# Kernel optimization log

Hardware: AMD Instinct MI355X
Metric: run time of the kernel (lower is better)

The kernel has to match this reference:

```python
import jax, jax.numpy as jnp
import numpy as np

N = 4096
FIN = 256
FOUT = 256
H = 1  # num_heads MUST be 1: edge projections reshape [N,N,H] -> (1,N,N)
NEG_MASK = -1000000.0
LRELU_SLOPE = 0.2
ESP = 1e-06
LN_EPS = 1e-05


def setup_inputs() -> dict:
    key = jax.random.key(0)
    ks = jax.random.split(key, 9)
    nodes_features = jax.random.normal(ks[0], (N, FIN), dtype=jnp.float32)
    degree_matrix = jax.random.normal(ks[1], (N, N), dtype=jnp.float32)
    edges_features_distance = jax.random.uniform(ks[2], (N, N), dtype=jnp.float32)
    edges_features_bond = jax.random.uniform(ks[3], (N, N), dtype=jnp.float32)
    # learned parameters (xavier-ish scale)
    proj_param = jax.random.normal(ks[4], (H, FIN, FOUT), dtype=jnp.float32) * (1.0 / np.sqrt(FIN))
    a_src = jax.random.normal(ks[5], (H, FOUT, 1), dtype=jnp.float32) * (1.0 / np.sqrt(FOUT))
    a_tgt = jax.random.normal(ks[6], (H, FOUT, 1), dtype=jnp.float32) * (1.0 / np.sqrt(FOUT))
    w_dist = jax.random.normal(ks[7], (H, 1), dtype=jnp.float32)  # nn.Linear(1, H).weight
    w_bond = jax.random.normal(ks[8], (H, 1), dtype=jnp.float32)
    return {
        "nodes_features": nodes_features,
        "degree_matrix": degree_matrix,
        "edges_features_distance": edges_features_distance,
        "edges_features_bond": edges_features_bond,
        "proj_param": proj_param,
        "a_src": a_src,
        "a_tgt": a_tgt,
        "w_dist": w_dist,
        "w_bond": w_bond,
        "cutoff": 0,
    }


def reference(nodes_features, degree_matrix, edges_features_distance,
              edges_features_bond, proj_param, a_src, a_tgt, w_dist, w_bond,
              cutoff=0):
    n = nodes_features.shape[0]
    h, fin, fout = proj_param.shape
    # connectivity mask: keep degree where positive, else large negative
    connectivity_mask = jnp.where(degree_matrix > 0, degree_matrix, NEG_MASK)
    # node projection: [H, N, Fout] (dropout is identity in eval)
    proj = jnp.einsum('nf,hfo->hno', nodes_features, proj_param)
    # attention scores: outer-sum of per-node source/target scores
    s_src = jnp.einsum('hno,hoi->hni', proj, a_src)      # [H, N, 1]
    s_tgt = jnp.einsum('hno,hoi->hni', proj, a_tgt)      # [H, N, 1]
    all_scores = jax.nn.leaky_relu(s_src + jnp.swapaxes(s_tgt, 1, 2), LRELU_SLOPE)  # [H,N,N]
    # edge contributions: Linear(1, H) on scalar edge features, reshaped (1,N,N) (H==1)
    dist_c = ((-edges_features_distance)[..., None] * w_dist[:, 0]).reshape(1, n, n)
    bond_c = (edges_features_bond[..., None] * w_bond[:, 0]).reshape(1, n, n)
    all_scores = all_scores + dist_c + bond_c
    # masked softmax over neighbors
    attn = jax.nn.softmax(all_scores + connectivity_mask[None], axis=-1)  # [H,N,N]
    # weighted aggregation
    out = jnp.einsum('hnm,hmo->hno', attn, proj)  # [H, N, Fout]
    # faithful to torch: transpose(2,1) -> [H,Fout,N] then contiguous view(-1,H,Fout)
    out = jnp.transpose(out, (0, 2, 1)).reshape(-1, h, fout)
    # concat heads (skip connection and bias are disabled per init args)
    out = out.reshape(-1, h * fout)
    out = jax.nn.elu(out)  # ELU activation, alpha=1
    # ---- no_grad connectivity update ----
    o = jax.lax.stop_gradient(out)
    dm = jax.lax.stop_gradient(degree_matrix)
    sim = o @ o.T                                        # [N, N]
    decay = -jax.lax.stop_gradient(edges_features_distance)
    upd = jax.nn.sigmoid(sim) * decay * (dm > 0).astype(o.dtype)
    upd = upd + ESP
    mean = jnp.mean(upd, axis=-1, keepdims=True)
    var = jnp.mean(jnp.square(upd - mean), axis=-1, keepdims=True)
    upd = (upd - mean) / jnp.sqrt(var + LN_EPS)          # layer_norm, no affine
    upd = upd + upd.T
    return out, upd
```

## Files before the change

kernel.cpp:

```cpp
#include <hip/hip_runtime.h>


using f32x4  = __attribute__((ext_vector_type(4))) float;
using bf16x8 = __attribute__((ext_vector_type(8))) __bf16;
using bf16x4 = __attribute__((ext_vector_type(4))) __bf16;
using u32x4  = __attribute__((ext_vector_type(4))) unsigned int;

__global__ __launch_bounds__(256) void cvt_nodes_kernel(const float* __restrict__ x,
                                                        __bf16* __restrict__ y) {
  int i = (blockIdx.x * 256 + threadIdx.x) * 4;
  f32x4 v = *(const f32x4*)(x + i);
  bf16x4 o = { (__bf16)v[0], (__bf16)v[1], (__bf16)v[2], (__bf16)v[3] };
  *(bf16x4*)(y + i) = o;
}

__global__ __launch_bounds__(256) void cvt_wt_kernel(const float* __restrict__ w,
                                                     __bf16* __restrict__ wt) {
  int i = blockIdx.x * 256 + threadIdx.x;
  int o = i >> 8, f = i & 255;
  wt[i] = (__bf16)w[f * 256 + o];
}

template<int BM, int BN, int MODE>
__global__ __launch_bounds__(256) void gemm_bf16_kernel(
    const __bf16* __restrict__ A, const __bf16* __restrict__ Bt,
    int M, int N, int K,
    float* __restrict__ outf, __bf16* __restrict__ outb,
    const float* __restrict__ e0, const float* __restrict__ e1,
    float* __restrict__ outt)
{
  constexpr int LDT = 72;
  constexpr int MI = BM / 32;
  constexpr int NI = BN / 32;
  __shared__ alignas(16) __bf16 As[BM * LDT];
  __shared__ alignas(16) __bf16 Bs[BN * LDT];
  const int tid  = threadIdx.x;
  const int lane = tid & 63;
  const int wid  = tid >> 6;
  const int wm0  = (wid >> 1) * (BM / 2);
  const int wn0  = (wid & 1) * (BN / 2);
  const int m0   = blockIdx.x * BM;
  const int n0   = blockIdx.y * BN;
  const int lr   = lane & 15;
  const int lk   = lane >> 4;

  f32x4 acc[MI][NI];
#pragma unroll
  for (int a = 0; a < MI; ++a)
#pragma unroll
    for (int b = 0; b < NI; ++b) acc[a][b] = (f32x4){0.f, 0.f, 0.f, 0.f};

  for (int kt = 0; kt < K; kt += 64) {
    __syncthreads();
    for (int idx = tid; idx < BM * 8; idx += 256) {
      int r = idx >> 3, c = idx & 7;
      u32x4 v = *(const u32x4*)(A + (size_t)(m0 + r) * K + kt + c * 8);
      *(u32x4*)(As + r * LDT + c * 8) = v;
    }
    for (int idx = tid; idx < BN * 8; idx += 256) {
      int r = idx >> 3, c = idx & 7;
      u32x4 v = *(const u32x4*)(Bt + (size_t)(n0 + r) * K + kt + c * 8);
      *(u32x4*)(Bs + r * LDT + c * 8) = v;
    }
    __syncthreads();
#pragma unroll
    for (int kk = 0; kk < 2; ++kk) {
      bf16x8 av[MI], bv[NI];
#pragma unroll
      for (int mi = 0; mi < MI; ++mi)
        av[mi] = *(const bf16x8*)(As + (wm0 + mi * 16 + lr) * LDT + kk * 32 + lk * 8);
#pragma unroll
      for (int ni = 0; ni < NI; ++ni)
        bv[ni] = *(const bf16x8*)(Bs + (wn0 + ni * 16 + lr) * LDT + kk * 32 + lk * 8);
#pragma unroll
      for (int mi = 0; mi < MI; ++mi)
#pragma unroll
        for (int ni = 0; ni < NI; ++ni)
          acc[mi][ni] = __builtin_amdgcn_mfma_f32_16x16x32_bf16(av[mi], bv[ni], acc[mi][ni], 0, 0, 0);
    }
  }

#pragma unroll
  for (int mi = 0; mi < MI; ++mi) {
#pragma unroll
    for (int ni = 0; ni < NI; ++ni) {
#pragma unroll
      for (int j = 0; j < 4; ++j) {
        const int m = m0 + wm0 + mi * 16 + lk * 4 + j;
        const int n = n0 + wn0 + ni * 16 + lr;
        const float v = acc[mi][ni][j];
        if constexpr (MODE == 0) {
          outf[(size_t)m * 256 + n] = v;
          outb[(size_t)n * 4096 + m] = (__bf16)v;
        } else {
          const size_t idx = (size_t)m * 4096 + n;
          const float d = e0[idx];
          const float g = e1[idx];
          const float s = 1.0f / (1.0f + expf(-v));
          outt[idx] = s * (-d) * (g > 0.f ? 1.0f : 0.0f) + 1e-6f;
        }
      }
    }
  }
}

__global__ __launch_bounds__(256) void gemm_splitk_kernel(
    const __bf16* __restrict__ A, const __bf16* __restrict__ Bt,
    float* __restrict__ partial)
{
  constexpr int LDT = 72;
  __shared__ alignas(16) __bf16 As[64 * LDT];
  __shared__ alignas(16) __bf16 Bs[64 * LDT];
  const int tid  = threadIdx.x;
  const int lane = tid & 63;
  const int wid  = tid >> 6;
  const int wm0  = (wid >> 1) * 32;
  const int wn0  = (wid & 1) * 32;
  const int m0   = blockIdx.x * 64;
  const int n0   = blockIdx.y * 64;
  const int s    = blockIdx.z;
  const int lr   = lane & 15;
  const int lk   = lane >> 4;

  f32x4 acc[2][2];
#pragma unroll
  for (int a = 0; a < 2; ++a)
#pragma unroll
    for (int b = 0; b < 2; ++b) acc[a][b] = (f32x4){0.f, 0.f, 0.f, 0.f};

  const int k0 = s * 512;
  for (int kt = k0; kt < k0 + 512; kt += 64) {
    __syncthreads();
    for (int idx = tid; idx < 512; idx += 256) {
      int r = idx >> 3, c = idx & 7;
      u32x4 v = *(const u32x4*)(A + (size_t)(m0 + r) * 4096 + kt + c * 8);
      *(u32x4*)(As + r * LDT + c * 8) = v;
    }
    for (int idx = tid; idx < 512; idx += 256) {
      int r = idx >> 3, c = idx & 7;
      u32x4 v = *(const u32x4*)(Bt + (size_t)(n0 + r) * 4096 + kt + c * 8);
      *(u32x4*)(Bs + r * LDT + c * 8) = v;
    }
    __syncthreads();
#pragma unroll
    for (int kk = 0; kk < 2; ++kk) {
      bf16x8 av[2], bv[2];
#pragma unroll
      for (int mi = 0; mi < 2; ++mi)
        av[mi] = *(const bf16x8*)(As + (wm0 + mi * 16 + lr) * LDT + kk * 32 + lk * 8);
#pragma unroll
      for (int ni = 0; ni < 2; ++ni)
        bv[ni] = *(const bf16x8*)(Bs + (wn0 + ni * 16 + lr) * LDT + kk * 32 + lk * 8);
#pragma unroll
      for (int mi = 0; mi < 2; ++mi)
#pragma unroll
        for (int ni = 0; ni < 2; ++ni)
          acc[mi][ni] = __builtin_amdgcn_mfma_f32_16x16x32_bf16(av[mi], bv[ni], acc[mi][ni], 0, 0, 0);
    }
  }

  float* P = partial + (size_t)s * (4096 * 256);
#pragma unroll
  for (int mi = 0; mi < 2; ++mi)
#pragma unroll
    for (int ni = 0; ni < 2; ++ni)
#pragma unroll
      for (int j = 0; j < 4; ++j) {
        const int m = m0 + wm0 + mi * 16 + lk * 4 + j;
        const int n = n0 + wn0 + ni * 16 + lr;
        P[(size_t)m * 256 + n] = acc[mi][ni][j];
      }
}

__global__ __launch_bounds__(256) void reduce_elu_kernel(
    const float* __restrict__ partial, float* __restrict__ out0,
    __bf16* __restrict__ E)
{
  __shared__ float tile[64][65];
  const int tid = threadIdx.x;
  const int m0 = blockIdx.x * 64;
  const int n0 = blockIdx.y * 64;
#pragma unroll
  for (int i = 0; i < 4; ++i) {
    int lin = i * 1024 + tid * 4;
    int r = lin >> 6, c = lin & 63;
    f32x4 sum = (f32x4){0.f, 0.f, 0.f, 0.f};
#pragma unroll
    for (int s = 0; s < 8; ++s)
      sum += *(const f32x4*)(partial + (size_t)s * (4096 * 256) +
                             (size_t)(m0 + r) * 256 + n0 + c);
    tile[r][c]     = sum[0];
    tile[r][c + 1] = sum[1];
    tile[r][c + 2] = sum[2];
    tile[r][c + 3] = sum[3];
  }
  __syncthreads();
#pragma unroll
  for (int i = 0; i < 4; ++i) {
    int lin = i * 1024 + tid * 4;
    int rr = lin >> 6, cc = lin & 63;
    f32x4 e;
#pragma unroll
    for (int q = 0; q < 4; ++q) {
      float v = tile[cc + q][rr];
      e[q] = v > 0.f ? v : expm1f(v);
    }
    size_t idx = (size_t)(n0 + rr) * 4096 + m0 + cc;
    *(f32x4*)(out0 + idx) = e;
    bf16x4 eb = { (__bf16)e[0], (__bf16)e[1], (__bf16)e[2], (__bf16)e[3] };
    *(bf16x4*)(E + idx) = eb;
  }
}

__global__ __launch_bounds__(256) void sproj_kernel(const float* __restrict__ proj,
                                                    const float* __restrict__ asrc,
                                                    const float* __restrict__ atgt,
                                                    float* __restrict__ ssrc,
                                                    float* __restrict__ stgt) {
  const int row  = blockIdx.x * 4 + (threadIdx.x >> 6);
  const int lane = threadIdx.x & 63;
  f32x4 p = *(const f32x4*)(proj + (size_t)row * 256 + lane * 4);
  f32x4 a = *(const f32x4*)(asrc + lane * 4);
  f32x4 b = *(const f32x4*)(atgt + lane * 4);
  float d1 = p[0]*a[0] + p[1]*a[1] + p[2]*a[2] + p[3]*a[3];
  float d2 = p[0]*b[0] + p[1]*b[1] + p[2]*b[2] + p[3]*b[3];
#pragma unroll
  for (int o = 32; o; o >>= 1) { d1 += __shfl_xor(d1, o, 64); d2 += __shfl_xor(d2, o, 64); }
  if (lane == 0) { ssrc[row] = d1; stgt[row] = d2; }
}

__global__ __launch_bounds__(256, 4) void scores_kernel(
    const float* __restrict__ dist, const float* __restrict__ bond,
    const float* __restrict__ deg,  const float* __restrict__ ssrc,
    const float* __restrict__ stgt, const float* __restrict__ wdp,
    const float* __restrict__ wbp,  __bf16* __restrict__ attn)
{
  const int row = blockIdx.x;
  const int tid = threadIdx.x;
  const float wd = wdp[0], wb = wbp[0];
  const float si = ssrc[row];
  const size_t base = (size_t)row * 4096;

  f32x4 st[4], d[4], b[4], g[4];
#pragma unroll
  for (int u = 0; u < 4; ++u) {
    const int j = u * 1024 + tid * 4;
    d[u]  = *(const f32x4*)(dist + base + j);
    g[u]  = *(const f32x4*)(deg  + base + j);
    b[u]  = *(const f32x4*)(bond + base + j);
    st[u] = *(const f32x4*)(stgt + j);
  }

  float sc[16];
  float vmax = -3.4e38f;
#pragma unroll
  for (int u = 0; u < 4; ++u) {
#pragma unroll
    for (int q = 0; q < 4; ++q) {
      float x = si + st[u][q];
      x = x > 0.f ? x : 0.2f * x;
      x += -d[u][q] * wd + b[u][q] * wb + (g[u][q] > 0.f ? g[u][q] : -1000000.0f);
      sc[u * 4 + q] = x;
      vmax = fmaxf(vmax, x);
    }
  }
#pragma unroll
  for (int o = 32; o; o >>= 1) vmax = fmaxf(vmax, __shfl_xor(vmax, o, 64));
  __shared__ float redm[4], reds[4];
  if ((tid & 63) == 0) redm[tid >> 6] = vmax;
  __syncthreads();
  vmax = fmaxf(fmaxf(redm[0], redm[1]), fmaxf(redm[2], redm[3]));
  float sum = 0.f;
#pragma unroll
  for (int i = 0; i < 16; ++i) { float e = expf(sc[i] - vmax); sc[i] = e; sum += e; }
#pragma unroll
  for (int o = 32; o; o >>= 1) sum += __shfl_xor(sum, o, 64);
  if ((tid & 63) == 0) reds[tid >> 6] = sum;
  __syncthreads();
  sum = reds[0] + reds[1] + reds[2] + reds[3];
  const float inv = 1.0f / sum;
#pragma unroll
  for (int u = 0; u < 4; ++u) {
    const int j = u * 1024 + tid * 4;
    bf16x4 o = { (__bf16)(sc[u*4+0] * inv), (__bf16)(sc[u*4+1] * inv),
                 (__bf16)(sc[u*4+2] * inv), (__bf16)(sc[u*4+3] * inv) };
    *(bf16x4*)(attn + base + j) = o;
  }
}

__global__ __launch_bounds__(256, 4) void stats_kernel(const float* __restrict__ t,
                                                       float* __restrict__ mean,
                                                       float* __restrict__ rstd) {
  const int row = blockIdx.x;
  const int tid = threadIdx.x;
  const float* tr = t + (size_t)row * 4096;
  f32x4 v[4];
#pragma unroll
  for (int u = 0; u < 4; ++u) v[u] = *(const f32x4*)(tr + u * 1024 + tid * 4);
  float s = 0.f, s2 = 0.f;
#pragma unroll
  for (int u = 0; u < 4; ++u)
#pragma unroll
    for (int q = 0; q < 4; ++q) { s += v[u][q]; s2 += v[u][q] * v[u][q]; }
#pragma unroll
  for (int o = 32; o; o >>= 1) { s += __shfl_xor(s, o, 64); s2 += __shfl_xor(s2, o, 64); }
  __shared__ float bs[4], bs2[4];
  if ((tid & 63) == 0) { bs[tid >> 6] = s; bs2[tid >> 6] = s2; }
  __syncthreads();
  if (tid == 0) {
    float S  = bs[0] + bs[1] + bs[2] + bs[3];
    float S2 = bs2[0] + bs2[1] + bs2[2] + bs2[3];
    float m  = S * (1.0f / 4096.0f);
    float var = S2 * (1.0f / 4096.0f) - m * m;
    mean[row] = m;
    rstd[row] = rsqrtf(var + 1e-5f);
  }
}

__global__ __launch_bounds__(256) void finalize_kernel(float* __restrict__ t,
                                                       const float* __restrict__ mean,
                                                       const float* __restrict__ rstd) {
  const int bj = blockIdx.x, bi = blockIdx.y;
  if (bi > bj) return;
  __shared__ float ta[64][65];
  __shared__ float tb[64][65];
  const int tid = threadIdx.x;
#pragma unroll
  for (int i = 0; i < 4; ++i) {
    int lin = i * 1024 + tid * 4;
    int r = lin >> 6, c = lin & 63;
    f32x4 va = *(const f32x4*)(t + (size_t)(bi * 64 + r) * 4096 + bj * 64 + c);
    ta[r][c] = va[0]; ta[r][c+1] = va[1]; ta[r][c+2] = va[2]; ta[r][c+3] = va[3];
  }
  if (bi != bj) {
#pragma unroll
    for (int i = 0; i < 4; ++i) {
      int lin = i * 1024 + tid * 4;
      int r = lin >> 6, c = lin & 63;
      f32x4 vb = *(const f32x4*)(t + (size_t)(bj * 64 + r) * 4096 + bi * 64 + c);
      tb[r][c] = vb[0]; tb[r][c+1] = vb[1]; tb[r][c+2] = vb[2]; tb[r][c+3] = vb[3];
    }
  }
  __syncthreads();
#pragma unroll
  for (int i = 0; i < 4; ++i) {
    int lin = i * 1024 + tid * 4;
    int r = lin >> 6, c = lin & 63;
    int gi = bi * 64 + r, gj = bj * 64 + c;
    const float mi_ = mean[gi], ri_ = rstd[gi];
    f32x4 mj = *(const f32x4*)(mean + gj);
    f32x4 rj = *(const f32x4*)(rstd + gj);
    f32x4 o;
#pragma unroll
    for (int q = 0; q < 4; ++q) {
      float v = (ta[r][c + q] - mi_) * ri_;
      float w = (bi == bj) ? (ta[c + q][r] - mj[q]) * rj[q]
                           : (tb[c + q][r] - mj[q]) * rj[q];
      o[q] = v + w;
    }
    *(f32x4*)(t + (size_t)gi * 4096 + gj) = o;
  }
  if (bi != bj) {
#pragma unroll
    for (int i = 0; i < 4; ++i) {
      int lin = i * 1024 + tid * 4;
      int r = lin >> 6, c = lin & 63;
      int gi = bj * 64 + r, gj = bi * 64 + c;
      const float mi_ = mean[gi], ri_ = rstd[gi];
      f32x4 mj = *(const f32x4*)(mean + gj);
      f32x4 rj = *(const f32x4*)(rstd + gj);
      f32x4 o;
#pragma unroll
      for (int q = 0; q < 4; ++q) {
        float v = (tb[r][c + q] - mi_) * ri_;
        float w = (ta[c + q][r] - mj[q]) * rj[q];
        o[q] = v + w;
      }
      *(f32x4*)(t + (size_t)gi * 4096 + gj) = o;
    }
  }
}

extern "C" void kernel_launch(void* const* d_in, const int* in_sizes, int n_in,
                              void* d_out, int out_size, void* d_ws, size_t ws_size,
                              hipStream_t stream) {
  const float* nodes  = (const float*)d_in[0];
  const float* degree = (const float*)d_in[1];
  const float* dist   = (const float*)d_in[2];
  const float* bond   = (const float*)d_in[3];
  const float* W      = (const float*)d_in[4];
  const float* a_src  = (const float*)d_in[5];
  const float* a_tgt  = (const float*)d_in[6];
  const float* w_dist = (const float*)d_in[7];
  const float* w_bond = (const float*)d_in[8];

  char* ws = (char*)d_ws;
  __bf16* nodesB = (__bf16*)ws;
  __bf16* Wt     = (__bf16*)(ws + (2u << 20));
  __bf16* projT  = (__bf16*)(ws + (2u << 20) + (256u << 10));
  float*  proj   = (float*)(ws + (5u << 20));
  __bf16* E      = (__bf16*)(ws + (9u << 20));
  float*  ssrc   = (float*)(ws + (11u << 20));
  float*  stgt   = ssrc + 4096;
  float*  mean   = stgt + 4096;
  float*  rstd   = mean + 4096;

  float*  out0 = (float*)d_out;
  float*  t    = out0 + (size_t)4096 * 256;
  __bf16* attn = (__bf16*)t;
  float*  partials = t + (size_t)4096 * 4096 / 2;

  cvt_nodes_kernel<<<1024, 256, 0, stream>>>(nodes, nodesB);
  cvt_wt_kernel<<<256, 256, 0, stream>>>(W, Wt);

  gemm_bf16_kernel<64, 64, 0><<<dim3(64, 4), 256, 0, stream>>>(
      nodesB, Wt, 4096, 256, 256, proj, projT, nullptr, nullptr, nullptr);

  sproj_kernel<<<1024, 256, 0, stream>>>(proj, a_src, a_tgt, ssrc, stgt);

  scores_kernel<<<4096, 256, 0, stream>>>(dist, bond, degree, ssrc, stgt,
                                          w_dist, w_bond, attn);

  gemm_splitk_kernel<<<dim3(64, 4, 8), 256, 0, stream>>>(attn, projT, partials);

  reduce_elu_kernel<<<dim3(64, 4), 256, 0, stream>>>(partials, out0, E);

  gemm_bf16_kernel<128, 128, 2><<<dim3(32, 32), 256, 0, stream>>>(
      E, E, 4096, 4096, 256, nullptr, nullptr, dist, degree, t);

  stats_kernel<<<4096, 256, 0, stream>>>(t, mean, rstd);

  finalize_kernel<<<dim3(64, 64), 256, 0, stream>>>(t, mean, rstd);
}
```

Measured before the change: 184.8 us.

## Precompute masked negative distance in bf16 during scores pass for similarity epilogue

The scores kernel, which already reads distance and degree, now also writes a bf16 auxiliary matrix holding -dist where degree>0 and 0 elsewhere. The similarity GEMM epilogue reads that single bf16 value instead of two fp32 matrices. This cuts epilogue read traffic from 8 to 2 bytes per element at the cost of a 2-byte-per-element write in the scores pass. The scores kernel is also reshaped to 1024 threads per row with one vector per thread. Storing the distance in bf16 adds rounding error to the update output.

```diff
diff --git a/kernel.cpp b/kernel.cpp
--- a/kernel.cpp
+++ b/kernel.cpp
@@ -27,7 +27,7 @@
     int M, int N, int K,
     float* __restrict__ outf, __bf16* __restrict__ outb,
     const float* __restrict__ e0, const float* __restrict__ e1,
-    float* __restrict__ outt)
+    const __bf16* __restrict__ axp, float* __restrict__ outt)
 {
   constexpr int LDT = 72;
   constexpr int MI = BM / 32;
@@ -92,12 +92,17 @@
         if constexpr (MODE == 0) {
           outf[(size_t)m * 256 + n] = v;
           outb[(size_t)n * 4096 + m] = (__bf16)v;
-        } else {
+        } else if constexpr (MODE == 2) {
           const size_t idx = (size_t)m * 4096 + n;
           const float d = e0[idx];
           const float g = e1[idx];
           const float s = 1.0f / (1.0f + expf(-v));
           outt[idx] = s * (-d) * (g > 0.f ? 1.0f : 0.0f) + 1e-6f;
+        } else {
+          const size_t idx = (size_t)m * 4096 + n;
+          const float a = (float)axp[idx];
+          const float s = 1.0f / (1.0f + expf(-v));
+          outt[idx] = s * a + 1e-6f;
         }
       }
     }
@@ -229,63 +234,63 @@
   if (lane == 0) { ssrc[row] = d1; stgt[row] = d2; }
 }
 
-__global__ __launch_bounds__(256, 4) void scores_kernel(
+__global__ __launch_bounds__(1024, 8) void scores_kernel(
     const float* __restrict__ dist, const float* __restrict__ bond,
     const float* __restrict__ deg,  const float* __restrict__ ssrc,
     const float* __restrict__ stgt, const float* __restrict__ wdp,
-    const float* __restrict__ wbp,  __bf16* __restrict__ attn)
+    const float* __restrict__ wbp,  __bf16* __restrict__ attn,
+    __bf16* __restrict__ aux)
 {
   const int row = blockIdx.x;
   const int tid = threadIdx.x;
+  const int wid = tid >> 6;
+  const int j   = tid * 4;
+  const size_t base = (size_t)row * 4096;
+
+  f32x4 d  = *(const f32x4*)(dist + base + j);
+  f32x4 g  = *(const f32x4*)(deg  + base + j);
+  f32x4 b  = *(const f32x4*)(bond + base + j);
+  f32x4 st = *(const f32x4*)(stgt + j);
   const float wd = wdp[0], wb = wbp[0];
   const float si = ssrc[row];
-  const size_t base = (size_t)row * 4096;
-
-  f32x4 st[4], d[4], b[4], g[4];
-#pragma unroll
-  for (int u = 0; u < 4; ++u) {
-    const int j = u * 1024 + tid * 4;
-    d[u]  = *(const f32x4*)(dist + base + j);
-    g[u]  = *(const f32x4*)(deg  + base + j);
-    b[u]  = *(const f32x4*)(bond + base + j);
-    st[u] = *(const f32x4*)(stgt + j);
-  }
-
-  float sc[16];
+
+  float sc[4];
+  bf16x4 ax;
   float vmax = -3.4e38f;
 #pragma unroll
-  for (int u = 0; u < 4; ++u) {
-#pragma unroll
-    for (int q = 0; q < 4; ++q) {
-      float x = si + st[u][q];
-      x = x > 0.f ? x : 0.2f * x;
-      x += -d[u][q] * wd + b[u][q] * wb + (g[u][q] > 0.f ? g[u][q] : -1000000.0f);
-      sc[u * 4 + q] = x;
-      vmax = fmaxf(vmax, x);
-    }
+  for (int q = 0; q < 4; ++q) {
+    float x = si + st[q];
+    x = x > 0.f ? x : 0.2f * x;
+    x += -d[q] * wd + b[q] * wb + (g[q] > 0.f ? g[q] : -1000000.0f);
+    sc[q] = x;
+    vmax = fmaxf(vmax, x);
+    ax[q] = (__bf16)(g[q] > 0.f ? -d[q] : 0.0f);
   }
 #pragma unroll
   for (int o = 32; o; o >>= 1) vmax = fmaxf(vmax, __shfl_xor(vmax, o, 64));
-  __shared__ float redm[4], reds[4];
-  if ((tid & 63) == 0) redm[tid >> 6] = vmax;
+  __shared__ float redm[16], reds[16];
+  if ((tid & 63) == 0) redm[wid] = vmax;
   __syncthreads();
-  vmax = fmaxf(fmaxf(redm[0], redm[1]), fmaxf(redm[2], redm[3]));
+  float vm = redm[0];
+#pragma unroll
+  for (int i = 1; i < 16; ++i) vm = fmaxf(vm, redm[i]);
+
   float sum = 0.f;
 #pragma unroll
-  for (int i = 0; i < 16; ++i) { float e = expf(sc[i] - vmax); sc[i] = e; sum += e; }
+  for (int q = 0; q < 4; ++q) { float e = expf(sc[q] - vm); sc[q] = e; sum += e; }
 #pragma unroll
   for (int o = 32; o; o >>= 1) sum += __shfl_xor(sum, o, 64);
-  if ((tid & 63) == 0) reds[tid >> 6] = sum;
+  if ((tid & 63) == 0) reds[wid] = sum;
   __syncthreads();
-  sum = reds[0] + reds[1] + reds[2] + reds[3];
-  const float inv = 1.0f / sum;
-#pragma unroll
-  for (int u = 0; u < 4; ++u) {
-    const int j = u * 1024 + tid * 4;
-    bf16x4 o = { (__bf16)(sc[u*4+0] * inv), (__bf16)(sc[u*4+1] * inv),
-                 (__bf16)(sc[u*4+2] * inv), (__bf16)(sc[u*4+3] * inv) };
-    *(bf16x4*)(attn + base + j) = o;
-  }
+  float S = 0.f;
+#pragma unroll
+  for (int i = 0; i < 16; ++i) S += reds[i];
+  const float inv = 1.0f / S;
+
+  bf16x4 o4 = { (__bf16)(sc[0] * inv), (__bf16)(sc[1] * inv),
+                (__bf16)(sc[2] * inv), (__bf16)(sc[3] * inv) };
+  *(bf16x4*)(attn + base + j) = o4;
+  if (aux) *(bf16x4*)(aux + base + j) = ax;
 }
 
 __global__ __launch_bounds__(256, 4) void stats_kernel(const float* __restrict__ t,
@@ -405,6 +410,9 @@
   float*  mean   = stgt + 4096;
   float*  rstd   = mean + 4096;
 
+  const bool useAux = ws_size >= (size_t)(44u << 20);
+  __bf16* aux = useAux ? (__bf16*)(ws + (12u << 20)) : nullptr;
+
   float*  out0 = (float*)d_out;
   float*  t    = out0 + (size_t)4096 * 256;
   __bf16* attn = (__bf16*)t;
@@ -414,19 +422,23 @@
   cvt_wt_kernel<<<256, 256, 0, stream>>>(W, Wt);
 
   gemm_bf16_kernel<64, 64, 0><<<dim3(64, 4), 256, 0, stream>>>(
-      nodesB, Wt, 4096, 256, 256, proj, projT, nullptr, nullptr, nullptr);
+      nodesB, Wt, 4096, 256, 256, proj, projT, nullptr, nullptr, nullptr, nullptr);
 
   sproj_kernel<<<1024, 256, 0, stream>>>(proj, a_src, a_tgt, ssrc, stgt);
 
-  scores_kernel<<<4096, 256, 0, stream>>>(dist, bond, degree, ssrc, stgt,
-                                          w_dist, w_bond, attn);
+  scores_kernel<<<4096, 1024, 0, stream>>>(dist, bond, degree, ssrc, stgt,
+                                           w_dist, w_bond, attn, aux);
 
   gemm_splitk_kernel<<<dim3(64, 4, 8), 256, 0, stream>>>(attn, projT, partials);
 
   reduce_elu_kernel<<<dim3(64, 4), 256, 0, stream>>>(partials, out0, E);
 
-  gemm_bf16_kernel<128, 128, 2><<<dim3(32, 32), 256, 0, stream>>>(
-      E, E, 4096, 4096, 256, nullptr, nullptr, dist, degree, t);
+  if (useAux)
+    gemm_bf16_kernel<128, 128, 3><<<dim3(32, 32), 256, 0, stream>>>(
+        E, E, 4096, 4096, 256, nullptr, nullptr, nullptr, nullptr, aux, t);
+  else
+    gemm_bf16_kernel<128, 128, 2><<<dim3(32, 32), 256, 0, stream>>>(
+        E, E, 4096, 4096, 256, nullptr, nullptr, dist, degree, nullptr, t);
 
   stats_kernel<<<4096, 256, 0, stream>>>(t, mean, rstd);
 
```

New measurement: 174.1 us. 1.06x faster.
